# Performance work log

Measured on AMD Instinct MI355X. Metric: run time of the kernel, lower is better.

The kernel has to match this reference:

```python
import jax, jax.numpy as jnp
import numpy as np

B, H, W, C = 16, 56, 56, 512
NUM_HEADS = 8
WS = 4  # window_size


def setup_inputs() -> dict:
    key = jax.random.key(0)
    k1, k2, k3, k4 = jax.random.split(key, 4)
    x = jax.random.normal(k1, (B, H, W, C), dtype=jnp.float32)
    w_qkv_h = jax.random.normal(k2, (3 * C, C), dtype=jnp.float32) * 0.02
    w_qkv_l = jax.random.normal(k3, (3 * C, C), dtype=jnp.float32) * 0.02
    w_proj = jax.random.normal(k4, (C, 2 * C), dtype=jnp.float32) * 0.02
    b_proj = jnp.zeros((C,), dtype=jnp.float32)
    return {"x": x, "w_qkv_h": w_qkv_h, "w_qkv_l": w_qkv_l,
            "w_proj": w_proj, "b_proj": b_proj}


def reference(x, w_qkv_h, w_qkv_l, w_proj, b_proj):
    b, h, w, c = x.shape
    nh = NUM_HEADS
    hd = c // nh
    nw = WS * WS  # tokens per window
    scale = c ** -0.5  # NOTE: original scales by full dim, not head dim

    # window partition: [B*H/ws*W/ws, ws*ws, C]
    xw = x.reshape(b, h // WS, WS, w // WS, WS, c)
    xw = xw.transpose(0, 1, 3, 2, 4, 5).reshape(-1, nw, c)

    # local branch qkv: [3, Nwin, nh, nw, hd]
    qkv_h = (xw @ w_qkv_h.T).reshape(-1, nw, 3, nh, hd).transpose(2, 0, 3, 1, 4)
    q_h, k_h, v_h = qkv_h[0], qkv_h[1], qkv_h[2]

    # global branch: average-pool each window to a single token [Nwin, 1, C]
    x_avg = x.reshape(b, h // WS, WS, w // WS, WS, c).mean(axis=(2, 4))
    x_avg = x_avg.reshape(-1, 1, c)
    qkv_l = (x_avg @ w_qkv_l.T).reshape(-1, 1, 3, nh, hd).transpose(2, 0, 3, 1, 4)
    q_l, k_l, v_l = qkv_l[0], qkv_l[1], qkv_l[2]

    # local window attention: [Nwin, nh, nw, nw]
    attn_h = jax.nn.softmax(jnp.einsum('bhqd,bhkd->bhqk', q_h, k_h) * scale, axis=-1)
    x_h = jnp.einsum('bhqk,bhkd->bhqd', attn_h, v_h)
    x_h = x_h.transpose(0, 2, 1, 3).reshape(-1, nw, c)

    # pooled global attention (1 token -> softmax over singleton = 1)
    attn_l = jax.nn.softmax(jnp.einsum('bhqd,bhkd->bhqk', q_l, k_l) * scale, axis=-1)
    x_l = jnp.einsum('bhqk,bhkd->bhqd', attn_l, v_l)
    x_l = x_l.transpose(0, 2, 1, 3).reshape(-1, 1, c)

    # concat local + broadcast global, project 2C -> C
    x_out = jnp.concatenate([x_h, jnp.broadcast_to(x_l, (x_l.shape[0], nw, c))], axis=-1)
    x_out = x_out @ w_proj.T + b_proj

    # window reverse
    x_out = x_out.reshape(b, h // WS, w // WS, WS, WS, c)
    x_out = x_out.transpose(0, 1, 3, 2, 4, 5).reshape(b, h, w, c)
    return x_out
```

## Files before the change

### kernel.cpp

```cpp
#include <hip/hip_runtime.h>


using bf16x8 = __attribute__((ext_vector_type(8))) short;
using f32x4  = __attribute__((ext_vector_type(4))) float;

#define SCALE 0.044194173824159216f

__device__ __forceinline__ unsigned short f2bf(float f) {
    union { float f; unsigned u; } v; v.f = f;
    unsigned u = v.u;
    return (unsigned short)((u + 0x7fffu + ((u >> 16) & 1u)) >> 16);
}

__device__ __forceinline__ void gl2lds16(const unsigned short* g, unsigned short* l) {
    __builtin_amdgcn_global_load_lds(
        (const __attribute__((address_space(1))) void*)g,
        (__attribute__((address_space(3))) void*)l, 16, 0, 0);
}

__global__ void k_prep_weights(const float* __restrict__ wqkv_h,
                               const float* __restrict__ wqkv_l,
                               const float* __restrict__ wproj,
                               unsigned short* __restrict__ WH,
                               unsigned short* __restrict__ WLV,
                               unsigned short* __restrict__ WP1,
                               unsigned short* __restrict__ WP2) {
    int i = blockIdx.x * 256 + threadIdx.x;
    if (i < 786432) {
        WH[i] = f2bf(wqkv_h[i]);
    } else {
        int j = i - 786432;
        int r = j >> 18;
        int t = j & 262143;
        int n = t >> 9, k = t & 511;
        if (r == 0)      WLV[t] = f2bf(wqkv_l[(1024 + n) * 512 + k]);
        else if (r == 1) WP1[t] = f2bf(wproj[n * 1024 + k]);
        else             WP2[t] = f2bf(wproj[n * 1024 + 512 + k]);
    }
}

__global__ void k_window_pool(const float* __restrict__ x,
                              unsigned short* __restrict__ XW,
                              unsigned short* __restrict__ XAVG) {
    int win = blockIdx.x * 2 + (threadIdx.x >> 7);
    int g = threadIdx.x & 127;
    int c = g * 4;
    int b = win / 196, rem = win % 196, wh = rem / 14, ww = rem % 14;
    float4 s = {0.f, 0.f, 0.f, 0.f};
    #pragma unroll
    for (int t = 0; t < 16; ++t) {
        int row = (b * 56 + wh * 4 + (t >> 2)) * 56 + ww * 4 + (t & 3);
        float4 v = *(const float4*)&x[(size_t)row * 512 + c];
        uint2 pk;
        pk.x = (unsigned)f2bf(v.x) | ((unsigned)f2bf(v.y) << 16);
        pk.y = (unsigned)f2bf(v.z) | ((unsigned)f2bf(v.w) << 16);
        *(uint2*)&XW[(size_t)(win * 16 + t) * 512 + c] = pk;
        s.x += v.x; s.y += v.y; s.z += v.z; s.w += v.w;
    }
    uint2 pa;
    pa.x = (unsigned)f2bf(s.x * 0.0625f) | ((unsigned)f2bf(s.y * 0.0625f) << 16);
    pa.y = (unsigned)f2bf(s.z * 0.0625f) | ((unsigned)f2bf(s.w * 0.0625f) << 16);
    *(uint2*)&XAVG[(size_t)win * 512 + c] = pa;
}

template <int NT>
__global__ void k_gemm512(const unsigned short* __restrict__ A,
                          const unsigned short* __restrict__ Bw,
                          unsigned short* __restrict__ outB,
                          float* __restrict__ outF,
                          const float* __restrict__ bias) {
    int wave = threadIdx.x >> 6, lane = threadIdx.x & 63;
    int quad = lane >> 4, l16 = lane & 15;
    int m0 = blockIdx.x * 64 + wave * 16;
    int n0 = blockIdx.y * (NT * 16);
    f32x4 acc[NT] = {};
    const unsigned short* arow = A + (size_t)(m0 + l16) * 512 + quad * 8;
    for (int kk = 0; kk < 16; ++kk) {
        bf16x8 a = *(const bf16x8*)(arow + kk * 32);
        #pragma unroll
        for (int nt = 0; nt < NT; ++nt) {
            bf16x8 b = *(const bf16x8*)(Bw + (size_t)(n0 + nt * 16 + l16) * 512 + kk * 32 + quad * 8);
            acc[nt] = __builtin_amdgcn_mfma_f32_16x16x32_bf16(a, b, acc[nt], 0, 0, 0);
        }
    }
    #pragma unroll
    for (int nt = 0; nt < NT; ++nt) {
        int col = n0 + nt * 16 + l16;
        float bv = (bias != nullptr) ? bias[col] : 0.f;
        #pragma unroll
        for (int r = 0; r < 4; ++r) {
            int row = m0 + quad * 4 + r;
            if (outF != nullptr) outF[(size_t)row * 512 + col] = acc[nt][r] + bv;
            else                 outB[(size_t)row * 512 + col] = f2bf(acc[nt][r]);
        }
    }
}

__global__ void __launch_bounds__(512, 2) k_fused(const unsigned short* __restrict__ XW,
                                                  const unsigned short* __restrict__ WH,
                                                  unsigned short* __restrict__ XH) {
    __shared__ __align__(16) char smem[131072];

    const int tid  = threadIdx.x;
    const int wave = tid >> 6, lane = tid & 63;
    const int quad = lane >> 4, l16 = lane & 15;
    const int mh = wave >> 1, nq = wave & 1;

    int id   = blockIdx.y * 196 + blockIdx.x;
    int w_   = (id & 7) * 196 + (id >> 3);
    int tb   = w_ >> 3, head = w_ & 7;
    const int m0 = tb * 256;

    int aof[4];
    #pragma unroll
    for (int i = 0; i < 4; ++i) {
        int u = i * 512 + tid;
        int n = u >> 3;
        int gu = (u & 7) ^ (n & 7);
        aof[i] = (m0 + n) * 512 + gu * 8;
    }
    int bof[3];
    #pragma unroll
    for (int i = 0; i < 3; ++i) {
        int u = i * 512 + tid;
        int n = u >> 3;
        int gu = (u & 7) ^ (n & 7);
        int nrow = (n >> 6) * 512 + head * 64 + (n & 63);
        bof[i] = nrow * 512 + gu * 8;
    }

    f32x4 acc[4][6] = {};
    const int sx = l16 & 7;

    {
        unsigned short* A0 = (unsigned short*)smem;
        unsigned short* B0 = (unsigned short*)(smem + 32768);
        #pragma unroll
        for (int i = 0; i < 4; ++i) gl2lds16(XW + aof[i], A0 + (i * 512 + wave * 64) * 8);
        #pragma unroll
        for (int i = 0; i < 3; ++i) gl2lds16(WH + bof[i], B0 + (i * 512 + wave * 64) * 8);
    }

    #pragma unroll
    for (int ch = 0; ch < 8; ++ch) {
        if (ch < 7) {
            unsigned short* An = (unsigned short*)(smem + ((ch + 1) & 1) * 57344);
            unsigned short* Bn = (unsigned short*)(smem + ((ch + 1) & 1) * 57344 + 32768);
            #pragma unroll
            for (int i = 0; i < 4; ++i) gl2lds16(XW + aof[i] + (ch + 1) * 64, An + (i * 512 + wave * 64) * 8);
            #pragma unroll
            for (int i = 0; i < 3; ++i) gl2lds16(WH + bof[i] + (ch + 1) * 64, Bn + (i * 512 + wave * 64) * 8);
        }
        if (ch < 7) asm volatile("s_waitcnt vmcnt(7)" ::: "memory");
        else        asm volatile("s_waitcnt vmcnt(0)" ::: "memory");
        __builtin_amdgcn_s_barrier();

        unsigned short* As = (unsigned short*)(smem + (ch & 1) * 57344);
        unsigned short* Bs = (unsigned short*)(smem + (ch & 1) * 57344 + 32768);
        #pragma unroll
        for (int kk = 0; kk < 2; ++kk) {
            int su = ((kk * 4 + quad) ^ sx) * 8;
            bf16x8 a[4], b[6];
            #pragma unroll
            for (int mf = 0; mf < 4; ++mf)
                a[mf] = *(const bf16x8*)&As[(mh * 64 + mf * 16 + l16) * 64 + su];
            #pragma unroll
            for (int j = 0; j < 6; ++j)
                b[j] = *(const bf16x8*)&Bs[(nq * 96 + j * 16 + l16) * 64 + su];
            #pragma unroll
            for (int mf = 0; mf < 4; ++mf)
                #pragma unroll
                for (int j = 0; j < 6; ++j)
                    acc[mf][j] = __builtin_amdgcn_mfma_f32_16x16x32_bf16(a[mf], b[j], acc[mf][j], 0, 0, 0);
        }
        asm volatile("s_waitcnt lgkmcnt(0)" ::: "memory");
        __builtin_amdgcn_s_barrier();
    }

    {
        char* att = smem + mh * 32768;
        unsigned short* qs  = (unsigned short*)att;
        unsigned short* ks  = (unsigned short*)(att + 9216);
        unsigned short* vts = (unsigned short*)(att + 18432);
        #pragma unroll
        for (int j = 0; j < 6; ++j) {
            int cb = nq * 96 + j * 16;
            #pragma unroll
            for (int mf = 0; mf < 4; ++mf) {
                #pragma unroll
                for (int r = 0; r < 4; ++r) {
                    int tok = mf * 16 + quad * 4 + r;
                    unsigned short hv = f2bf(acc[mf][j][r]);
                    if (cb < 64)       qs[tok * 72 + cb + l16] = hv;
                    else if (cb < 128) ks[tok * 72 + (cb - 64) + l16] = hv;
                    else               vts[(cb - 128 + l16) * 80 + tok] = hv;
                }
            }
        }
    }
    __syncthreads();

    char* att = smem + (wave >> 1) * 32768;
    unsigned short* qs  = (unsigned short*)att;
    unsigned short* ks  = (unsigned short*)(att + 9216);
    unsigned short* vts = (unsigned short*)(att + 18432);
    unsigned short* Ps  = (unsigned short*)(att + 28672);
    const int set = wave >> 1;

    #pragma unroll
    for (int sub = 0; sub < 2; ++sub) {
        const int lw = (wave & 1) * 2 + sub;
        const int t0 = lw * 16;

        if (lw == 3) {
            #pragma unroll
            for (int i = 0; i < 16; ++i) vts[lane * 80 + 64 + i] = 0;
        }
        {
            int prow = lane >> 2, pc = 16 + (lane & 3) * 4;
            #pragma unroll
            for (int i = 0; i < 4; ++i) Ps[lw * 512 + prow * 32 + pc + i] = 0;
        }

        f32x4 sacc = {};
        {
            bf16x8 a0 = *(const bf16x8*)&qs[(t0 + l16) * 72 + quad * 8];
            bf16x8 b0 = *(const bf16x8*)&ks[(t0 + l16) * 72 + quad * 8];
            sacc = __builtin_amdgcn_mfma_f32_16x16x32_bf16(a0, b0, sacc, 0, 0, 0);
            bf16x8 a1 = *(const bf16x8*)&qs[(t0 + l16) * 72 + 32 + quad * 8];
            bf16x8 b1 = *(const bf16x8*)&ks[(t0 + l16) * 72 + 32 + quad * 8];
            sacc = __builtin_amdgcn_mfma_f32_16x16x32_bf16(a1, b1, sacc, 0, 0, 0);
        }
        float p[4];
        #pragma unroll
        for (int r = 0; r < 4; ++r) {
            float v = sacc[r] * SCALE;
            float m = v;
            m = fmaxf(m, __shfl_xor(m, 1));
            m = fmaxf(m, __shfl_xor(m, 2));
            m = fmaxf(m, __shfl_xor(m, 4));
            m = fmaxf(m, __shfl_xor(m, 8));
            float e = __expf(v - m);
            float sm = e;
            sm += __shfl_xor(sm, 1);
            sm += __shfl_xor(sm, 2);
            sm += __shfl_xor(sm, 4);
            sm += __shfl_xor(sm, 8);
            p[r] = e / sm;
        }
        #pragma unroll
        for (int r = 0; r < 4; ++r)
            Ps[lw * 512 + (quad * 4 + r) * 32 + l16] = f2bf(p[r]);

        bf16x8 pa = *(const bf16x8*)&Ps[lw * 512 + l16 * 32 + quad * 8];
        #pragma unroll
        for (int nt = 0; nt < 4; ++nt) {
            f32x4 y = {};
            bf16x8 bv = *(const bf16x8*)&vts[(nt * 16 + l16) * 80 + t0 + quad * 8];
            y = __builtin_amdgcn_mfma_f32_16x16x32_bf16(pa, bv, y, 0, 0, 0);
            #pragma unroll
            for (int r = 0; r < 4; ++r)
                XH[(size_t)(m0 + set * 64 + t0 + quad * 4 + r) * 512 + head * 64 + nt * 16 + l16] = f2bf(y[r]);
        }
    }
}

__global__ void __launch_bounds__(256, 2) k_gemm_proj(const unsigned short* __restrict__ XH,
                                                      const unsigned short* __restrict__ WP1,
                                                      const float* __restrict__ G,
                                                      float* __restrict__ out) {
    __shared__ __align__(16) char smem[65536];

    const int wave = threadIdx.x >> 6, lane = threadIdx.x & 63;
    const int quad = lane >> 4, l16 = lane & 15;

    int id = blockIdx.y * 392 + blockIdx.x;
    int s  = id >> 3;
    int xb = (id & 7) * 49 + (s >> 2);
    int yb = s & 3;
    const int m0 = xb * 128, n0 = yb * 128;
    const int wm = (wave >> 1) * 64;
    const int wn = (wave & 1) * 64;

    int aofs[4], bofs[4];
    #pragma unroll
    for (int i = 0; i < 4; ++i) {
        int u = (wave * 4 + i) * 64 + lane;
        int n = u >> 3;
        int gu = (lane & 7) ^ (n & 7);
        aofs[i] = (m0 + n) * 512 + gu * 8;
        bofs[i] = (n0 + n) * 512 + gu * 8;
    }

    unsigned short* const bufA[2] = { (unsigned short*)smem,
                                      (unsigned short*)(smem + 32768) };
    unsigned short* const bufB[2] = { (unsigned short*)(smem + 16384),
                                      (unsigned short*)(smem + 32768 + 16384) };

    f32x4 acc[4][4] = {};
    const int sx = l16 & 7;

    #pragma unroll
    for (int i = 0; i < 4; ++i) {
        gl2lds16(XH + aofs[i], bufA[0] + (wave * 4 + i) * 512);
        gl2lds16(WP1 + bofs[i], bufB[0] + (wave * 4 + i) * 512);
    }

    #pragma unroll
    for (int ch = 0; ch < 8; ++ch) {
        if (ch < 7) {
            unsigned short* An = bufA[(ch + 1) & 1];
            unsigned short* Bn = bufB[(ch + 1) & 1];
            #pragma unroll
            for (int i = 0; i < 4; ++i) {
                gl2lds16(XH + aofs[i] + (ch + 1) * 64, An + (wave * 4 + i) * 512);
                gl2lds16(WP1 + bofs[i] + (ch + 1) * 64, Bn + (wave * 4 + i) * 512);
            }
        }
        if (ch < 7) asm volatile("s_waitcnt vmcnt(8)" ::: "memory");
        else        asm volatile("s_waitcnt vmcnt(0)" ::: "memory");
        __builtin_amdgcn_s_barrier();

        unsigned short* As = bufA[ch & 1];
        unsigned short* Bs = bufB[ch & 1];
        #pragma unroll
        for (int kk = 0; kk < 2; ++kk) {
            int su = ((kk * 4 + quad) ^ sx) * 8;
            bf16x8 a[4], b[4];
            #pragma unroll
            for (int mf = 0; mf < 4; ++mf)
                a[mf] = *(const bf16x8*)&As[(wm + mf * 16 + l16) * 64 + su];
            #pragma unroll
            for (int j = 0; j < 4; ++j)
                b[j] = *(const bf16x8*)&Bs[(wn + j * 16 + l16) * 64 + su];
            #pragma unroll
            for (int mf = 0; mf < 4; ++mf)
                #pragma unroll
                for (int j = 0; j < 4; ++j)
                    acc[mf][j] = __builtin_amdgcn_mfma_f32_16x16x32_bf16(a[mf], b[j], acc[mf][j], 0, 0, 0);
        }
        asm volatile("s_waitcnt lgkmcnt(0)" ::: "memory");
        __builtin_amdgcn_s_barrier();
    }

    #pragma unroll
    for (int mf = 0; mf < 4; ++mf) {
        #pragma unroll
        for (int r = 0; r < 4; ++r) {
            int tl  = wm + mf * 16 + quad * 4 + r;
            int gt  = m0 + tl;
            int win = gt >> 4, tw = gt & 15;
            int bb = win / 196, rem = win % 196;
            int wh = rem / 14, ww = rem % 14;
            int orow = (bb * 56 + wh * 4 + (tw >> 2)) * 56 + ww * 4 + (tw & 3);
            #pragma unroll
            for (int j = 0; j < 4; ++j) {
                int ncol = n0 + wn + j * 16 + l16;
                out[(size_t)orow * 512 + ncol] = acc[mf][j][r] + G[(size_t)win * 512 + ncol];
            }
        }
    }
}

extern "C" void kernel_launch(void* const* d_in, const int* in_sizes, int n_in,
                              void* d_out, int out_size, void* d_ws, size_t ws_size,
                              hipStream_t stream) {
    const float* x      = (const float*)d_in[0];
    const float* wqkv_h = (const float*)d_in[1];
    const float* wqkv_l = (const float*)d_in[2];
    const float* wproj  = (const float*)d_in[3];
    const float* bproj  = (const float*)d_in[4];
    float* out = (float*)d_out;

    char* ws = (char*)d_ws;
    unsigned short* WH   = (unsigned short*)(ws + 0);
    unsigned short* WLV  = (unsigned short*)(ws + 1572864);
    unsigned short* WP1  = (unsigned short*)(ws + 2097152);
    unsigned short* WP2  = (unsigned short*)(ws + 2621440);
    unsigned short* XW   = (unsigned short*)(ws + 3145728);
    unsigned short* XAVG = (unsigned short*)(ws + 54525952);
    unsigned short* VL   = (unsigned short*)(ws + 57737216);
    float*          G    = (float*)(ws + 60948480);
    unsigned short* XH   = (unsigned short*)(ws + 67371008);

    k_prep_weights<<<dim3(6144), dim3(256), 0, stream>>>(wqkv_h, wqkv_l, wproj, WH, WLV, WP1, WP2);
    k_window_pool<<<dim3(1568), dim3(256), 0, stream>>>(x, XW, XAVG);
    k_gemm512<2><<<dim3(49, 16), dim3(256), 0, stream>>>(XAVG, WLV, VL, (float*)nullptr, (const float*)nullptr);
    k_gemm512<2><<<dim3(49, 16), dim3(256), 0, stream>>>(VL, WP2, (unsigned short*)nullptr, G, bproj);
    k_fused<<<dim3(196, 8), dim3(512), 0, stream>>>(XW, WH, XH);
    k_gemm_proj<<<dim3(392, 4), dim3(256), 0, stream>>>(XH, WP1, G, out);
}
```

Measured before the change: 390.3 us.

## Fuse window partition and pooling into the fused QKV-attention kernel

Removes the separate window-pool kernel and the bf16 XW intermediate. The fused kernel now reads fp32 x directly through registers, converts it to bf16 into a single LDS A buffer, and emits the pooled window average from the head-0 blocks. LDS drops from 128KB to 80KB, and the attention epilogue runs in two passes so the smaller buffer can be reused. The cost is that each of the 8 head blocks re-reads fp32 x, which doubles the activation read bytes per block relative to reading bf16. A single-buffered A tile also serializes its stores against the MFMA reads.

```diff
diff --git a/kernel.cpp b/kernel.cpp
--- a/kernel.cpp
+++ b/kernel.cpp
@@ -10,6 +10,10 @@
     union { float f; unsigned u; } v; v.f = f;
     unsigned u = v.u;
     return (unsigned short)((u + 0x7fffu + ((u >> 16) & 1u)) >> 16);
+}
+
+__device__ __forceinline__ unsigned pk2(float a, float b) {
+    return (unsigned)f2bf(a) | ((unsigned)f2bf(b) << 16);
 }
 
 __device__ __forceinline__ void gl2lds16(const unsigned short* g, unsigned short* l) {
@@ -39,30 +43,6 @@
     }
 }
 
-__global__ void k_window_pool(const float* __restrict__ x,
-                              unsigned short* __restrict__ XW,
-                              unsigned short* __restrict__ XAVG) {
-    int win = blockIdx.x * 2 + (threadIdx.x >> 7);
-    int g = threadIdx.x & 127;
-    int c = g * 4;
-    int b = win / 196, rem = win % 196, wh = rem / 14, ww = rem % 14;
-    float4 s = {0.f, 0.f, 0.f, 0.f};
-    #pragma unroll
-    for (int t = 0; t < 16; ++t) {
-        int row = (b * 56 + wh * 4 + (t >> 2)) * 56 + ww * 4 + (t & 3);
-        float4 v = *(const float4*)&x[(size_t)row * 512 + c];
-        uint2 pk;
-        pk.x = (unsigned)f2bf(v.x) | ((unsigned)f2bf(v.y) << 16);
-        pk.y = (unsigned)f2bf(v.z) | ((unsigned)f2bf(v.w) << 16);
-        *(uint2*)&XW[(size_t)(win * 16 + t) * 512 + c] = pk;
-        s.x += v.x; s.y += v.y; s.z += v.z; s.w += v.w;
-    }
-    uint2 pa;
-    pa.x = (unsigned)f2bf(s.x * 0.0625f) | ((unsigned)f2bf(s.y * 0.0625f) << 16);
-    pa.y = (unsigned)f2bf(s.z * 0.0625f) | ((unsigned)f2bf(s.w * 0.0625f) << 16);
-    *(uint2*)&XAVG[(size_t)win * 512 + c] = pa;
-}
-
 template <int NT>
 __global__ void k_gemm512(const unsigned short* __restrict__ A,
                           const unsigned short* __restrict__ Bw,
@@ -96,10 +76,45 @@
     }
 }
 
-__global__ void __launch_bounds__(512, 2) k_fused(const unsigned short* __restrict__ XW,
+__device__ __forceinline__ void st_row(unsigned short* Ab, int wofs, float4 v0, float4 v1) {
+    uint4 pk;
+    pk.x = pk2(v0.x, v0.y); pk.y = pk2(v0.z, v0.w);
+    pk.z = pk2(v1.x, v1.y); pk.w = pk2(v1.z, v1.w);
+    *(uint4*)&Ab[wofs] = pk;
+}
+
+__device__ __forceinline__ void xavg_emit(const float4 (&xc)[4][2], int sg,
+                                          unsigned short* __restrict__ XAVG,
+                                          size_t dofs) {
+    float v[8];
+    v[0] = xc[0][0].x + xc[1][0].x + xc[2][0].x + xc[3][0].x;
+    v[1] = xc[0][0].y + xc[1][0].y + xc[2][0].y + xc[3][0].y;
+    v[2] = xc[0][0].z + xc[1][0].z + xc[2][0].z + xc[3][0].z;
+    v[3] = xc[0][0].w + xc[1][0].w + xc[2][0].w + xc[3][0].w;
+    v[4] = xc[0][1].x + xc[1][1].x + xc[2][1].x + xc[3][1].x;
+    v[5] = xc[0][1].y + xc[1][1].y + xc[2][1].y + xc[3][1].y;
+    v[6] = xc[0][1].z + xc[1][1].z + xc[2][1].z + xc[3][1].z;
+    v[7] = xc[0][1].w + xc[1][1].w + xc[2][1].w + xc[3][1].w;
+    #pragma unroll
+    for (int c = 0; c < 8; ++c) {
+        v[c] += __shfl_xor(v[c], 8);
+        v[c] += __shfl_xor(v[c], 16);
+    }
+    if (sg == 0) {
+        uint4 pa;
+        pa.x = pk2(v[0] * 0.0625f, v[1] * 0.0625f);
+        pa.y = pk2(v[2] * 0.0625f, v[3] * 0.0625f);
+        pa.z = pk2(v[4] * 0.0625f, v[5] * 0.0625f);
+        pa.w = pk2(v[6] * 0.0625f, v[7] * 0.0625f);
+        *(uint4*)&XAVG[dofs] = pa;
+    }
+}
+
+__global__ void __launch_bounds__(512, 2) k_fused(const float* __restrict__ x,
                                                   const unsigned short* __restrict__ WH,
-                                                  unsigned short* __restrict__ XH) {
-    __shared__ __align__(16) char smem[131072];
+                                                  unsigned short* __restrict__ XH,
+                                                  unsigned short* __restrict__ XAVG) {
+    __shared__ __align__(16) char smem[81920];
 
     const int tid  = threadIdx.x;
     const int wave = tid >> 6, lane = tid & 63;
@@ -111,14 +126,19 @@
     int tb   = w_ >> 3, head = w_ & 7;
     const int m0 = tb * 256;
 
-    int aof[4];
-    #pragma unroll
-    for (int i = 0; i < 4; ++i) {
-        int u = i * 512 + tid;
-        int n = u >> 3;
-        int gu = (u & 7) ^ (n & 7);
-        aof[i] = (m0 + n) * 512 + gu * 8;
-    }
+    const int sw = tid >> 5, sg = (tid >> 3) & 3, ss = tid & 7;
+    const int win_g = tb * 16 + sw;
+    int bb = win_g / 196, rem = win_g % 196, wh = rem / 14, ww = rem % 14;
+    const float* xbase = x + (size_t)(((bb * 56 + wh * 4 + sg) * 56 + ww * 4) * 512) + ss * 8;
+    int wofs0, wofs1, wofs2, wofs3;
+    {
+        int r0 = 16 * sw + 4 * sg;
+        wofs0 = (r0 + 0) * 64 + ((ss ^ ((r0 + 0) & 7)) * 8);
+        wofs1 = (r0 + 1) * 64 + ((ss ^ ((r0 + 1) & 7)) * 8);
+        wofs2 = (r0 + 2) * 64 + ((ss ^ ((r0 + 2) & 7)) * 8);
+        wofs3 = (r0 + 3) * 64 + ((ss ^ ((r0 + 3) & 7)) * 8);
+    }
+
     int bof[3];
     #pragma unroll
     for (int i = 0; i < 3; ++i) {
@@ -132,136 +152,161 @@
     f32x4 acc[4][6] = {};
     const int sx = l16 & 7;
 
+    float4 xrA[4][2], xrB[4][2];
+
+    #pragma unroll
+    for (int j = 0; j < 4; ++j) {
+        xrA[j][0] = *(const float4*)(xbase + (size_t)j * 512);
+        xrA[j][1] = *(const float4*)(xbase + (size_t)j * 512 + 4);
+    }
     {
-        unsigned short* A0 = (unsigned short*)smem;
         unsigned short* B0 = (unsigned short*)(smem + 32768);
         #pragma unroll
-        for (int i = 0; i < 4; ++i) gl2lds16(XW + aof[i], A0 + (i * 512 + wave * 64) * 8);
-        #pragma unroll
-        for (int i = 0; i < 3; ++i) gl2lds16(WH + bof[i], B0 + (i * 512 + wave * 64) * 8);
-    }
-
-    #pragma unroll
-    for (int ch = 0; ch < 8; ++ch) {
-        if (ch < 7) {
-            unsigned short* An = (unsigned short*)(smem + ((ch + 1) & 1) * 57344);
-            unsigned short* Bn = (unsigned short*)(smem + ((ch + 1) & 1) * 57344 + 32768);
-            #pragma unroll
-            for (int i = 0; i < 4; ++i) gl2lds16(XW + aof[i] + (ch + 1) * 64, An + (i * 512 + wave * 64) * 8);
-            #pragma unroll
-            for (int i = 0; i < 3; ++i) gl2lds16(WH + bof[i] + (ch + 1) * 64, Bn + (i * 512 + wave * 64) * 8);
-        }
-        if (ch < 7) asm volatile("s_waitcnt vmcnt(7)" ::: "memory");
-        else        asm volatile("s_waitcnt vmcnt(0)" ::: "memory");
-        __builtin_amdgcn_s_barrier();
-
-        unsigned short* As = (unsigned short*)(smem + (ch & 1) * 57344);
-        unsigned short* Bs = (unsigned short*)(smem + (ch & 1) * 57344 + 32768);
-        #pragma unroll
-        for (int kk = 0; kk < 2; ++kk) {
-            int su = ((kk * 4 + quad) ^ sx) * 8;
-            bf16x8 a[4], b[6];
-            #pragma unroll
-            for (int mf = 0; mf < 4; ++mf)
-                a[mf] = *(const bf16x8*)&As[(mh * 64 + mf * 16 + l16) * 64 + su];
-            #pragma unroll
-            for (int j = 0; j < 6; ++j)
-                b[j] = *(const bf16x8*)&Bs[(nq * 96 + j * 16 + l16) * 64 + su];
-            #pragma unroll
-            for (int mf = 0; mf < 4; ++mf)
-                #pragma unroll
-                for (int j = 0; j < 6; ++j)
-                    acc[mf][j] = __builtin_amdgcn_mfma_f32_16x16x32_bf16(a[mf], b[j], acc[mf][j], 0, 0, 0);
-        }
-        asm volatile("s_waitcnt lgkmcnt(0)" ::: "memory");
-        __builtin_amdgcn_s_barrier();
-    }
-
-    {
-        char* att = smem + mh * 32768;
+        for (int i = 0; i < 3; ++i)
+            gl2lds16(WH + bof[i], B0 + (i * 512 + wave * 64) * 8);
+    }
+
+#define QKV_STEP(CH, XRC, XRN)                                                 \
+{                                                                              \
+    unsigned short* Ab = (unsigned short*)smem;                                \
+    unsigned short* Bb = (unsigned short*)(smem + 32768 + ((CH) & 1) * 24576); \
+              \
+    st_row(Ab, wofs0, XRC[0][0], XRC[0][1]);                                   \
+    st_row(Ab, wofs1, XRC[1][0], XRC[1][1]);                                   \
+    st_row(Ab, wofs2, XRC[2][0], XRC[2][1]);                                   \
+    st_row(Ab, wofs3, XRC[3][0], XRC[3][1]);                                   \
+    if (head == 0)                                                             \
+        xavg_emit(XRC, sg, XAVG, (size_t)win_g * 512 + (CH) * 64 + ss * 8);    \
+    if ((CH) < 7) {                                                            \
+        _Pragma("unroll")                                                      \
+        for (int j = 0; j < 4; ++j) {                                          \
+            XRN[j][0] = *(const float4*)(xbase + (size_t)j * 512 + ((CH) + 1) * 64);     \
+            XRN[j][1] = *(const float4*)(xbase + (size_t)j * 512 + ((CH) + 1) * 64 + 4); \
+        }                                                                      \
+        unsigned short* Bn = (unsigned short*)(smem + 32768 + (((CH) + 1) & 1) * 24576); \
+        _Pragma("unroll")                                                      \
+        for (int i = 0; i < 3; ++i)                                            \
+            gl2lds16(WH + bof[i] + ((CH) + 1) * 64, Bn + (i * 512 + wave * 64) * 8);     \
+        asm volatile("s_waitcnt vmcnt(11)" ::: "memory");                      \
+    } else {                                                                   \
+        asm volatile("s_waitcnt vmcnt(0)" ::: "memory");                       \
+    }                                                                          \
+    asm volatile("s_waitcnt lgkmcnt(0)" ::: "memory");                         \
+    __builtin_amdgcn_s_barrier();                                              \
+    _Pragma("unroll")                                                          \
+    for (int kk = 0; kk < 2; ++kk) {                                           \
+        int su = ((kk * 4 + quad) ^ sx) * 8;                                   \
+        bf16x8 a[4], b[6];                                                     \
+        _Pragma("unroll")                                                      \
+        for (int mf = 0; mf < 4; ++mf)                                         \
+            a[mf] = *(const bf16x8*)&Ab[(mh * 64 + mf * 16 + l16) * 64 + su];  \
+        _Pragma("unroll")                                                      \
+        for (int j = 0; j < 6; ++j)                                            \
+            b[j] = *(const bf16x8*)&Bb[(nq * 96 + j * 16 + l16) * 64 + su];    \
+        _Pragma("unroll")                                                      \
+        for (int mf = 0; mf < 4; ++mf)                                         \
+            _Pragma("unroll")                                                  \
+            for (int j = 0; j < 6; ++j)                                        \
+                acc[mf][j] = __builtin_amdgcn_mfma_f32_16x16x32_bf16(a[mf], b[j], acc[mf][j], 0, 0, 0); \
+    }                                                                          \
+    asm volatile("s_waitcnt lgkmcnt(0)" ::: "memory");                         \
+    __builtin_amdgcn_s_barrier();                                              \
+}
+
+    QKV_STEP(0, xrA, xrB)
+    QKV_STEP(1, xrB, xrA)
+    QKV_STEP(2, xrA, xrB)
+    QKV_STEP(3, xrB, xrA)
+    QKV_STEP(4, xrA, xrB)
+    QKV_STEP(5, xrB, xrA)
+    QKV_STEP(6, xrA, xrB)
+    QKV_STEP(7, xrB, xrA)
+#undef QKV_STEP
+
+    #pragma unroll
+    for (int pass = 0; pass < 2; ++pass) {
+        const int active = (mh >> 1) == pass;
+        char* att = smem + (mh & 1) * 32768;
         unsigned short* qs  = (unsigned short*)att;
         unsigned short* ks  = (unsigned short*)(att + 9216);
         unsigned short* vts = (unsigned short*)(att + 18432);
-        #pragma unroll
-        for (int j = 0; j < 6; ++j) {
-            int cb = nq * 96 + j * 16;
-            #pragma unroll
-            for (int mf = 0; mf < 4; ++mf) {
+        unsigned short* Ps  = (unsigned short*)(att + 28672);
+
+        if (active) {
+            #pragma unroll
+            for (int j = 0; j < 6; ++j) {
+                int cb = nq * 96 + j * 16;
+                #pragma unroll
+                for (int mf = 0; mf < 4; ++mf) {
+                    #pragma unroll
+                    for (int r = 0; r < 4; ++r) {
+                        int tok = mf * 16 + quad * 4 + r;
+                        unsigned short hv = f2bf(acc[mf][j][r]);
+                        if (cb < 64)       qs[tok * 72 + cb + l16] = hv;
+                        else if (cb < 128) ks[tok * 72 + (cb - 64) + l16] = hv;
+                        else               vts[(cb - 128 + l16) * 80 + tok] = hv;
+                    }
+                }
+            }
+        }
+        __syncthreads();
+
+        if (active) {
+            #pragma unroll
+            for (int sub = 0; sub < 2; ++sub) {
+                const int lw = nq * 2 + sub;
+                const int t0 = lw * 16;
+                if (lw == 3) {
+                    #pragma unroll
+                    for (int i = 0; i < 16; ++i) vts[lane * 80 + 64 + i] = 0;
+                }
+                {
+                    int prow = lane >> 2, pc = 16 + (lane & 3) * 4;
+                    #pragma unroll
+                    for (int i = 0; i < 4; ++i) Ps[lw * 512 + prow * 32 + pc + i] = 0;
+                }
+                f32x4 sacc = {};
+                {
+                    bf16x8 a0 = *(const bf16x8*)&qs[(t0 + l16) * 72 + quad * 8];
+                    bf16x8 b0 = *(const bf16x8*)&ks[(t0 + l16) * 72 + quad * 8];
+                    sacc = __builtin_amdgcn_mfma_f32_16x16x32_bf16(a0, b0, sacc, 0, 0, 0);
+                    bf16x8 a1 = *(const bf16x8*)&qs[(t0 + l16) * 72 + 32 + quad * 8];
+                    bf16x8 b1 = *(const bf16x8*)&ks[(t0 + l16) * 72 + 32 + quad * 8];
+                    sacc = __builtin_amdgcn_mfma_f32_16x16x32_bf16(a1, b1, sacc, 0, 0, 0);
+                }
+                float p[4];
                 #pragma unroll
                 for (int r = 0; r < 4; ++r) {
-                    int tok = mf * 16 + quad * 4 + r;
-                    unsigned short hv = f2bf(acc[mf][j][r]);
-                    if (cb < 64)       qs[tok * 72 + cb + l16] = hv;
-                    else if (cb < 128) ks[tok * 72 + (cb - 64) + l16] = hv;
-                    else               vts[(cb - 128 + l16) * 80 + tok] = hv;
+                    float v = sacc[r] * SCALE;
+                    float m = v;
+                    m = fmaxf(m, __shfl_xor(m, 1));
+                    m = fmaxf(m, __shfl_xor(m, 2));
+                    m = fmaxf(m, __shfl_xor(m, 4));
+                    m = fmaxf(m, __shfl_xor(m, 8));
+                    float e = __expf(v - m);
+                    float sm = e;
+                    sm += __shfl_xor(sm, 1);
+                    sm += __shfl_xor(sm, 2);
+                    sm += __shfl_xor(sm, 4);
+                    sm += __shfl_xor(sm, 8);
+                    p[r] = e / sm;
+                }
+                #pragma unroll
+                for (int r = 0; r < 4; ++r)
+                    Ps[lw * 512 + (quad * 4 + r) * 32 + l16] = f2bf(p[r]);
+                bf16x8 pa = *(const bf16x8*)&Ps[lw * 512 + l16 * 32 + quad * 8];
+                #pragma unroll
+                for (int nt = 0; nt < 4; ++nt) {
+                    f32x4 y = {};
+                    bf16x8 bv = *(const bf16x8*)&vts[(nt * 16 + l16) * 80 + t0 + quad * 8];
+                    y = __builtin_amdgcn_mfma_f32_16x16x32_bf16(pa, bv, y, 0, 0, 0);
+                    #pragma unroll
+                    for (int r = 0; r < 4; ++r)
+                        XH[(size_t)(m0 + mh * 64 + t0 + quad * 4 + r) * 512 + head * 64 + nt * 16 + l16] = f2bf(y[r]);
                 }
             }
         }
-    }
-    __syncthreads();
-
-    char* att = smem + (wave >> 1) * 32768;
-    unsigned short* qs  = (unsigned short*)att;
-    unsigned short* ks  = (unsigned short*)(att + 9216);
-    unsigned short* vts = (unsigned short*)(att + 18432);
-    unsigned short* Ps  = (unsigned short*)(att + 28672);
-    const int set = wave >> 1;
-
-    #pragma unroll
-    for (int sub = 0; sub < 2; ++sub) {
-        const int lw = (wave & 1) * 2 + sub;
-        const int t0 = lw * 16;
-
-        if (lw == 3) {
-            #pragma unroll
-            for (int i = 0; i < 16; ++i) vts[lane * 80 + 64 + i] = 0;
-        }
-        {
-            int prow = lane >> 2, pc = 16 + (lane & 3) * 4;
-            #pragma unroll
-            for (int i = 0; i < 4; ++i) Ps[lw * 512 + prow * 32 + pc + i] = 0;
-        }
-
-        f32x4 sacc = {};
-        {
-            bf16x8 a0 = *(const bf16x8*)&qs[(t0 + l16) * 72 + quad * 8];
-            bf16x8 b0 = *(const bf16x8*)&ks[(t0 + l16) * 72 + quad * 8];
-            sacc = __builtin_amdgcn_mfma_f32_16x16x32_bf16(a0, b0, sacc, 0, 0, 0);
-            bf16x8 a1 = *(const bf16x8*)&qs[(t0 + l16) * 72 + 32 + quad * 8];
-            bf16x8 b1 = *(const bf16x8*)&ks[(t0 + l16) * 72 + 32 + quad * 8];
-            sacc = __builtin_amdgcn_mfma_f32_16x16x32_bf16(a1, b1, sacc, 0, 0, 0);
-        }
-        float p[4];
-        #pragma unroll
-        for (int r = 0; r < 4; ++r) {
-            float v = sacc[r] * SCALE;
-            float m = v;
-            m = fmaxf(m, __shfl_xor(m, 1));
-            m = fmaxf(m, __shfl_xor(m, 2));
-            m = fmaxf(m, __shfl_xor(m, 4));
-            m = fmaxf(m, __shfl_xor(m, 8));
-            float e = __expf(v - m);
-            float sm = e;
-            sm += __shfl_xor(sm, 1);
-            sm += __shfl_xor(sm, 2);
-            sm += __shfl_xor(sm, 4);
-            sm += __shfl_xor(sm, 8);
-            p[r] = e / sm;
-        }
-        #pragma unroll
-        for (int r = 0; r < 4; ++r)
-            Ps[lw * 512 + (quad * 4 + r) * 32 + l16] = f2bf(p[r]);
-
-        bf16x8 pa = *(const bf16x8*)&Ps[lw * 512 + l16 * 32 + quad * 8];
-        #pragma unroll
-        for (int nt = 0; nt < 4; ++nt) {
-            f32x4 y = {};
-            bf16x8 bv = *(const bf16x8*)&vts[(nt * 16 + l16) * 80 + t0 + quad * 8];
-            y = __builtin_amdgcn_mfma_f32_16x16x32_bf16(pa, bv, y, 0, 0, 0);
-            #pragma unroll
-            for (int r = 0; r < 4; ++r)
-                XH[(size_t)(m0 + set * 64 + t0 + quad * 4 + r) * 512 + head * 64 + nt * 16 + l16] = f2bf(y[r]);
-        }
+        __syncthreads();
     }
 }
 
@@ -377,16 +422,14 @@
     unsigned short* WLV  = (unsigned short*)(ws + 1572864);
     unsigned short* WP1  = (unsigned short*)(ws + 2097152);
     unsigned short* WP2  = (unsigned short*)(ws + 2621440);
-    unsigned short* XW   = (unsigned short*)(ws + 3145728);
     unsigned short* XAVG = (unsigned short*)(ws + 54525952);
     unsigned short* VL   = (unsigned short*)(ws + 57737216);
     float*          G    = (float*)(ws + 60948480);
     unsigned short* XH   = (unsigned short*)(ws + 67371008);
 
     k_prep_weights<<<dim3(6144), dim3(256), 0, stream>>>(wqkv_h, wqkv_l, wproj, WH, WLV, WP1, WP2);
-    k_window_pool<<<dim3(1568), dim3(256), 0, stream>>>(x, XW, XAVG);
+    k_fused<<<dim3(196, 8), dim3(512), 0, stream>>>(x, WH, XH, XAVG);
     k_gemm512<2><<<dim3(49, 16), dim3(256), 0, stream>>>(XAVG, WLV, VL, (float*)nullptr, (const float*)nullptr);
     k_gemm512<2><<<dim3(49, 16), dim3(256), 0, stream>>>(VL, WP2, (unsigned short*)nullptr, G, bproj);
-    k_fused<<<dim3(196, 8), dim3(512), 0, stream>>>(XW, WH, XH);
     k_gemm_proj<<<dim3(392, 4), dim3(256), 0, stream>>>(XH, WP1, G, out);
 }
```

After: 443.6 us. +13.7%, slower.
